# Optimization experiments

Measured on AMD Instinct MI355X. Metric: run time of the kernel, lower is better.

The kernel has to match this reference:

```python
import jax, jax.numpy as jnp
import numpy as np

N_NODES = 100000


def _gcn_norm(edge_index, num_nodes):
    """Add self-loops and compute symmetric GCN normalization coefficients.
    Returns (src, dst, norm) for the augmented edge list."""
    loop = jnp.arange(num_nodes, dtype=edge_index.dtype)
    src = jnp.concatenate([edge_index[0], loop])
    dst = jnp.concatenate([edge_index[1], loop])
    deg = jax.ops.segment_sum(jnp.ones_like(src, dtype=jnp.float32), dst,
                              num_segments=num_nodes)
    dinv = jnp.where(deg > 0, jax.lax.rsqrt(deg), 0.0)
    norm = dinv[src] * dinv[dst]  # [E + N]
    return src, dst, norm


def setup_inputs() -> dict:
    key = jax.random.key(0)
    ks = jax.random.split(key, 7)
    d = 64
    E = 1000000
    x = jax.random.normal(ks[0], (N_NODES, d), dtype=jnp.float32)
    edge_index = jax.random.randint(ks[1], (2, E), 0, N_NODES, dtype=jnp.int64)
    s = 1.0 / np.sqrt(d)
    Ws = jax.random.normal(ks[2], (3, d, d), dtype=jnp.float32) * s
    bs = jax.random.normal(ks[3], (3, d), dtype=jnp.float32) * 0.02
    W_out = jax.random.normal(ks[4], (d, d), dtype=jnp.float32) * s
    b_out = jax.random.normal(ks[5], (d,), dtype=jnp.float32) * 0.02
    return {"x": x, "edge_index": edge_index, "Ws": Ws, "bs": bs,
            "W_out": W_out, "b_out": b_out}


def reference(x, edge_index, Ws, bs, W_out, b_out):
    num_nodes = x.shape[0]
    src, dst, norm = _gcn_norm(edge_index, num_nodes)  # fixed graph -> compute once
    for i in range(Ws.shape[0]):  # small fixed layer count
        h = x @ Ws[i]                              # [N, d] linear transform
        msg = norm[:, None] * h[src]               # gather + scale  [E+N, d]
        x = jax.ops.segment_sum(msg, dst, num_segments=num_nodes) + bs[i]
        x = jax.nn.relu(x)
    return x @ W_out + b_out
```

## Files before the change

kernel.cpp:

```cpp
#include <hip/hip_runtime.h>
#include <hip/hip_bf16.h>

#define D 64
#define BSHIFT 8
#define BNODES 256
#define BCAP 4096
#define PTILE 2048

typedef __attribute__((ext_vector_type(8))) short short8;
typedef __attribute__((ext_vector_type(4))) float float4v;


__device__ __forceinline__ float bf16u_to_f32(unsigned short u) {
  union { unsigned int i; float f; } c;
  c.i = ((unsigned int)u) << 16;
  return c.f;
}

__device__ __forceinline__ unsigned short f32_to_bf16u(float f) {
  union { float f; unsigned int u; } c;
  c.f = f;
  unsigned int r = (c.u + 0x7fffu + ((c.u >> 16) & 1u)) >> 16;
  return (unsigned short)r;
}


__global__ void k_probe(const void* W, const void* ei, int* flags) {
  int lane = threadIdx.x & 63;
  const unsigned short* wb = (const unsigned short*)W;
  bool big = false;
  for (int i = lane; i < 512; i += 64) {
    float v = bf16u_to_f32(wb[i]);
    if (!(fabsf(v) < 100.f)) big = true;
  }
  int anybig = __any(big);
  const int* e32 = (const int*)ei;
  bool nz = (e32[2 * lane + 1] != 0);
  int anynz = __any(nz);
  if (threadIdx.x == 0) {
    flags[0] = anybig ? 1 : 0;
    flags[1] = anynz ? 0 : 1;
  }
}


__global__ __launch_bounds__(256) void k_prep(
    const void* __restrict__ Ws, const void* __restrict__ Wout,
    const void* __restrict__ bs, const void* __restrict__ bout,
    const int* __restrict__ flags, unsigned short* __restrict__ WT,
    float* __restrict__ biasf, int* __restrict__ bucket_cursor) {
  int f32 = flags[0];
  int gid = blockIdx.x * 256 + threadIdx.x;
  int stride = gridDim.x * 256;

  for (int i = gid; i < 512; i += stride) bucket_cursor[i] = i * BCAP;

  for (int i = gid; i < 4 * 4096; i += stride) {
    int l = i >> 12;
    int r = i & 4095;
    int k = r >> 6;
    int nn = r & 63;
    unsigned short v;
    if (l < 3) {
      v = f32 ? f32_to_bf16u(((const float*)Ws)[l * 4096 + r])
              : ((const unsigned short*)Ws)[l * 4096 + r];
    } else {
      v = f32 ? f32_to_bf16u(((const float*)Wout)[r])
              : ((const unsigned short*)Wout)[r];
    }
    WT[l * 4096 + nn * 64 + k] = v;
  }
  for (int i = gid; i < 4 * 64; i += stride) {
    int l = i >> 6;
    int j = i & 63;
    float v;
    if (l < 3)
      v = f32 ? ((const float*)bs)[l * 64 + j]
              : bf16u_to_f32(((const unsigned short*)bs)[l * 64 + j]);
    else
      v = f32 ? ((const float*)bout)[j]
              : bf16u_to_f32(((const unsigned short*)bout)[j]);
    biasf[i] = v;
  }
}


__global__ __launch_bounds__(256) void k_partition(
    const void* __restrict__ ei, const int* __restrict__ flags,
    int* __restrict__ bucket_cursor, int* __restrict__ packed, int e) {
  __shared__ int lhist[512];
  __shared__ int lbase[512];
  int tid = threadIdx.x;
  int t0 = blockIdx.x * PTILE;
  int tend = min(t0 + PTILE, e);
  if (t0 >= e) return;
  int i64 = flags[1];

  for (int b = tid; b < 512; b += 256) lhist[b] = 0;
  __syncthreads();

  if (i64) {
    const long long* dst = (const long long*)ei + e;
    for (int i = t0 + tid; i < tend; i += 256)
      atomicAdd(&lhist[((int)dst[i]) >> BSHIFT], 1);
  } else {
    const int* dst = (const int*)ei + e;
    for (int i = t0 + tid; i < tend; i += 256)
      atomicAdd(&lhist[dst[i] >> BSHIFT], 1);
  }
  __syncthreads();

  for (int b = tid; b < 512; b += 256) {
    int c = lhist[b];
    lbase[b] = c ? atomicAdd(&bucket_cursor[b], c) : 0;
    lhist[b] = 0;
  }
  __syncthreads();

  if (i64) {
    const long long* srcp = (const long long*)ei;
    const long long* dstp = srcp + e;
    for (int i = t0 + tid; i < tend; i += 256) {
      int s = (int)srcp[i];
      int d = (int)dstp[i];
      int b = d >> BSHIFT;
      int r = atomicAdd(&lhist[b], 1);
      packed[lbase[b] + r] = (s << BSHIFT) | (d & (BNODES - 1));
    }
  } else {
    const int* srcp = (const int*)ei;
    const int* dstp = srcp + e;
    for (int i = t0 + tid; i < tend; i += 256) {
      int s = srcp[i];
      int d = dstp[i];
      int b = d >> BSHIFT;
      int r = atomicAdd(&lhist[b], 1);
      packed[lbase[b] + r] = (s << BSHIFT) | (d & (BNODES - 1));
    }
  }
}

__global__ __launch_bounds__(256) void k_sort_csr(
    const int* __restrict__ packed, const int* __restrict__ bucket_cursor,
    int* __restrict__ csr, int2* __restrict__ rowrange,
    float* __restrict__ dinv, int n) {
  __shared__ int lcnt[BNODES];
  __shared__ int lofs[BNODES];
  __shared__ int sbuf[BNODES];
  int tid = threadIdx.x;
  int bucket = blockIdx.x;
  int node0 = bucket << BSHIFT;
  int nodes = min(BNODES, n - node0);
  int s0 = bucket * BCAP;
  int s1 = bucket_cursor[bucket];
  lcnt[tid] = 0;
  __syncthreads();
  for (int i = s0 + tid; i < s1; i += 256)
    atomicAdd(&lcnt[packed[i] & (BNODES - 1)], 1);
  __syncthreads();
  int v = lcnt[tid];
  sbuf[tid] = v;
  __syncthreads();
  for (int off = 1; off < BNODES; off <<= 1) {
    int tv = (tid >= off) ? sbuf[tid - off] : 0;
    __syncthreads();
    sbuf[tid] += tv;
    __syncthreads();
  }
  int excl = sbuf[tid] - v;
  lofs[tid] = excl;
  lcnt[tid] = 0;
  if (tid < nodes) {
    rowrange[node0 + tid] = make_int2(s0 + excl, s0 + excl + v);
    dinv[node0 + tid] = rsqrtf((float)(v + 1));
  }
  __syncthreads();
  for (int i = s0 + tid; i < s1; i += 256) {
    int pk = packed[i];
    int ld = pk & (BNODES - 1);
    int r = atomicAdd(&lcnt[ld], 1);
    csr[s0 + lofs[ld] + r] = pk >> BSHIFT;
  }
}


__global__ __launch_bounds__(256) void k_scale(
    const void* __restrict__ x0, const int* __restrict__ flags,
    const float* __restrict__ dinv, ushort4* __restrict__ z, int n16) {
  int f32 = flags[0];
  int i = blockIdx.x * 256 + threadIdx.x;
  int stride = gridDim.x * 256;
  for (; i < n16; i += stride) {
    float d = dinv[i >> 4];
    ushort4 o;
    if (f32) {
      float4 v = ((const float4*)x0)[i];
      o.x = f32_to_bf16u(d * v.x);
      o.y = f32_to_bf16u(d * v.y);
      o.z = f32_to_bf16u(d * v.z);
      o.w = f32_to_bf16u(d * v.w);
    } else {
      ushort4 v = ((const ushort4*)x0)[i];
      o.x = f32_to_bf16u(d * bf16u_to_f32(v.x));
      o.y = f32_to_bf16u(d * bf16u_to_f32(v.y));
      o.z = f32_to_bf16u(d * bf16u_to_f32(v.z));
      o.w = f32_to_bf16u(d * bf16u_to_f32(v.w));
    }
    z[i] = o;
  }
}

__global__ __launch_bounds__(256, 4) void k_fused(
    const unsigned short* __restrict__ z, const int2* __restrict__ rowrange,
    const int* __restrict__ csr, const float* __restrict__ dinv,
    const unsigned short* __restrict__ WT, const float* __restrict__ biasf,
    unsigned short* __restrict__ out, int n, int scale_out) {
  __shared__ unsigned short ybf[16 * 80];
  int tid = threadIdx.x;
  int lane = tid & 63;
  int w = tid >> 6;
  int q = lane >> 4;
  int f = lane & 15;
  int h = lane & 7;
  int g8 = lane >> 3;

  short8 b0 = *(const short8*)(WT + (size_t)(f + 16 * w) * 64 + q * 8);
  short8 b1 = *(const short8*)(WT + (size_t)(f + 16 * w) * 64 + 32 + q * 8);

  int row0 = blockIdx.x * 16;
  int base_node = row0 + w * 4;
  const short8* z8 = (const short8*)z;

  int rrw = 0;
  if (lane < 8) rrw = ((const int*)rowrange)[(size_t)base_node * 2 + lane];
  int rx0 = __shfl(rrw, 0, 64);
  int ry0 = __shfl(rrw, 1, 64);
  int rx1 = __shfl(rrw, 2, 64);
  int ry1 = __shfl(rrw, 3, 64);
  int rx2 = __shfl(rrw, 4, 64);
  int ry2 = __shfl(rrw, 5, 64);
  int rx3 = __shfl(rrw, 6, 64);
  int ry3 = __shfl(rrw, 7, 64);
  int deg0 = ry0 - rx0;
  int deg1 = ry1 - rx1;
  int deg2 = ry2 - rx2;
  int deg3 = ry3 - rx3;

  int jx = lane >> 4;
  int m = lane & 15;
  int rxj = (jx & 2) ? ((jx & 1) ? rx3 : rx2) : ((jx & 1) ? rx1 : rx0);
  int dgj = (jx & 2) ? ((jx & 1) ? deg3 : deg2) : ((jx & 1) ? deg1 : deg0);
  int coff = (m >= 1 && m <= dgj) ? (m - 1) : 0;
  int idx = csr[rxj + coff];
  if (m == 0) idx = base_node + jx;

  float ac[4][4][2];
  float a0[8] = {0, 0, 0, 0, 0, 0, 0, 0};
  float a1[8] = {0, 0, 0, 0, 0, 0, 0, 0};
  float a2[8] = {0, 0, 0, 0, 0, 0, 0, 0};
  float a3[8] = {0, 0, 0, 0, 0, 0, 0, 0};
  (void)ac;

  short8 g[8];
#pragma unroll
  for (int t = 0; t < 8; t++) {
    int u = ((t & 1) << 3) + g8;
    int sl = ((t >> 1) << 4) + u;
    int s = __shfl(idx, sl, 64);
    g[t] = z8[(size_t)s * 8 + h];
  }
#pragma unroll
  for (int t = 0; t < 8; t++) {
    int u = ((t & 1) << 3) + g8;
    const int j = t >> 1;
    int dg = (j == 0) ? deg0 : (j == 1) ? deg1 : (j == 2) ? deg2 : deg3;
    float vm = (u <= dg) ? 1.f : 0.f;
    float* aj = (j == 0) ? a0 : (j == 1) ? a1 : (j == 2) ? a2 : a3;
#pragma unroll
    for (int c = 0; c < 8; c++)
      aj[c] += vm * bf16u_to_f32((unsigned short)g[t][c]);
  }

#pragma unroll
  for (int j = 0; j < 4; j++) {
    int rx = (j == 0) ? rx0 : (j == 1) ? rx1 : (j == 2) ? rx2 : rx3;
    int dg = (j == 0) ? deg0 : (j == 1) ? deg1 : (j == 2) ? deg2 : deg3;
    float* aj = (j == 0) ? a0 : (j == 1) ? a1 : (j == 2) ? a2 : a3;
    for (int e0 = 15; e0 < dg; e0 += 8) {
      int e = e0 + g8;
      bool vv = e < dg;
      int s = csr[rx + (vv ? e : 0)];
      short8 tv = z8[(size_t)s * 8 + h];
      float vm = vv ? 1.f : 0.f;
#pragma unroll
      for (int c = 0; c < 8; c++)
        aj[c] += vm * bf16u_to_f32((unsigned short)tv[c]);
    }
  }

#pragma unroll
  for (int c = 0; c < 8; c++) {
    a0[c] += __shfl_xor(a0[c], 8, 64);
    a1[c] += __shfl_xor(a1[c], 8, 64);
    a2[c] += __shfl_xor(a2[c], 8, 64);
    a3[c] += __shfl_xor(a3[c], 8, 64);
    a0[c] += __shfl_xor(a0[c], 16, 64);
    a1[c] += __shfl_xor(a1[c], 16, 64);
    a2[c] += __shfl_xor(a2[c], 16, 64);
    a3[c] += __shfl_xor(a3[c], 16, 64);
    a0[c] += __shfl_xor(a0[c], 32, 64);
    a1[c] += __shfl_xor(a1[c], 32, 64);
    a2[c] += __shfl_xor(a2[c], 32, 64);
    a3[c] += __shfl_xor(a3[c], 32, 64);
  }

  if (lane < 32) {
    int jw = lane >> 3;
    float dv = dinv[base_node + jw];
    unsigned int pk[4];
#pragma unroll
    for (int cp = 0; cp < 4; cp++) {
      float vlo = (jw & 2) ? ((jw & 1) ? a3[2 * cp] : a2[2 * cp])
                           : ((jw & 1) ? a1[2 * cp] : a0[2 * cp]);
      float vhi = (jw & 2) ? ((jw & 1) ? a3[2 * cp + 1] : a2[2 * cp + 1])
                           : ((jw & 1) ? a1[2 * cp + 1] : a0[2 * cp + 1]);
      unsigned int lo = f32_to_bf16u(dv * vlo);
      unsigned int hi = f32_to_bf16u(dv * vhi);
      pk[cp] = lo | (hi << 16);
    }
    *(uint4*)&ybf[(w * 4 + jw) * 80 + 8 * h] =
        make_uint4(pk[0], pk[1], pk[2], pk[3]);
  }
  __syncthreads();

  short8 fa0 = *(const short8*)&ybf[f * 80 + q * 8];
  short8 fa1 = *(const short8*)&ybf[f * 80 + 32 + q * 8];
  float4v zz = {0.f, 0.f, 0.f, 0.f};
  float4v acc = __builtin_amdgcn_mfma_f32_16x16x32_bf16(fa0, b0, zz, 0, 0, 0);
  acc = __builtin_amdgcn_mfma_f32_16x16x32_bf16(fa1, b1, acc, 0, 0, 0);

  float bv = biasf[16 * w + f];
  if (scale_out) {
    float4 dv4 = *(const float4*)(dinv + row0 + q * 4);
    float d[4] = {dv4.x, dv4.y, dv4.z, dv4.w};
#pragma unroll
    for (int reg = 0; reg < 4; reg++) {
      int row = row0 + q * 4 + reg;
      if (row < n)
        out[(size_t)row * 64 + 16 * w + f] =
            f32_to_bf16u(d[reg] * fmaxf(acc[reg] + bv, 0.f));
    }
  } else {
#pragma unroll
    for (int reg = 0; reg < 4; reg++) {
      int row = row0 + q * 4 + reg;
      if (row < n)
        out[(size_t)row * 64 + 16 * w + f] =
            f32_to_bf16u(fmaxf(acc[reg] + bv, 0.f));
    }
  }
}

__global__ __launch_bounds__(256) void k_gemm_final(
    const unsigned short* __restrict__ xin,
    const unsigned short* __restrict__ WT, const float* __restrict__ bias,
    void* __restrict__ out, const int* __restrict__ flags, int ntiles) {
  int lane = threadIdx.x & 63;
  int wid = threadIdx.x >> 6;
  int f = lane & 15;
  int q = lane >> 4;

  short8 bfr[4][2];
#pragma unroll
  for (int ct = 0; ct < 4; ct++)
#pragma unroll
    for (int kt = 0; kt < 2; kt++)
      bfr[ct][kt] =
          *(const short8*)(WT + (size_t)(f + 16 * ct) * 64 + kt * 32 + q * 8);

  int wave = blockIdx.x * 4 + wid;
  int nwaves = gridDim.x * 4;
  for (int t = wave; t < ntiles; t += nwaves) {
    int row0 = t * 16;
    const unsigned short* xr = xin + (size_t)(row0 + f) * 64 + q * 8;
    short8 a0 = *(const short8*)(xr);
    short8 a1 = *(const short8*)(xr + 32);
    float4v acc[4];
#pragma unroll
    for (int ct = 0; ct < 4; ct++) {
      float4v z = {0.f, 0.f, 0.f, 0.f};
      acc[ct] =
          __builtin_amdgcn_mfma_f32_16x16x32_bf16(a0, bfr[ct][0], z, 0, 0, 0);
      acc[ct] = __builtin_amdgcn_mfma_f32_16x16x32_bf16(a1, bfr[ct][1],
                                                        acc[ct], 0, 0, 0);
    }
    int f32o = flags[0];
    float bv[4];
#pragma unroll
    for (int ct = 0; ct < 4; ct++) bv[ct] = bias[f + 16 * ct];
    if (f32o) {
      float* op = (float*)out;
#pragma unroll
      for (int reg = 0; reg < 4; reg++) {
        size_t rb = (size_t)(row0 + q * 4 + reg) * 64 + f;
#pragma unroll
        for (int ct = 0; ct < 4; ct++) op[rb + 16 * ct] = acc[ct][reg] + bv[ct];
      }
    } else {
      unsigned short* op = (unsigned short*)out;
#pragma unroll
      for (int reg = 0; reg < 4; reg++) {
        size_t rb = (size_t)(row0 + q * 4 + reg) * 64 + f;
#pragma unroll
        for (int ct = 0; ct < 4; ct++)
          op[rb + 16 * ct] = f32_to_bf16u(acc[ct][reg] + bv[ct]);
      }
    }
  }
}


extern "C" void kernel_launch(void* const* d_in, const int* in_sizes, int n_in,
                              void* d_out, int out_size, void* d_ws,
                              size_t ws_size, hipStream_t stream) {
  const void* x0 = d_in[0];
  const void* ei = d_in[1];
  const void* Ws = d_in[2];
  const void* bs = d_in[3];
  const void* Wout = d_in[4];
  const void* bout = d_in[5];

  const int N = in_sizes[0] / D;
  const int E = in_sizes[1] / 2;
  const int NBUC = (N + BNODES - 1) >> BSHIFT;
  const int NT = (N + 15) / 16;

  char* p = (char*)d_ws;
  auto alloc = [&](size_t bytes) {
    char* r = p;
    p += (bytes + 511) & ~(size_t)511;
    return r;
  };
  int* flags = (int*)alloc(8);
  int* bucket_cursor = (int*)alloc(512 * 4);
  int* packed = (int*)alloc((size_t)512 * BCAP * 4);
  int* csr = (int*)alloc((size_t)512 * BCAP * 4);
  int2* rowrange = (int2*)alloc((size_t)N * 8);
  float* dinv = (float*)alloc((size_t)N * 4);
  unsigned short* WT = (unsigned short*)alloc(4 * 4096 * 2);
  float* biasf = (float*)alloc(4 * 64 * 4);
  unsigned short* za = (unsigned short*)alloc((size_t)N * D * 2);
  unsigned short* zb = (unsigned short*)alloc((size_t)N * D * 2);
  (void)ws_size;
  (void)n_in;
  (void)out_size;

  k_probe<<<1, 64, 0, stream>>>(Ws, ei, flags);
  k_prep<<<32, 256, 0, stream>>>(Ws, Wout, bs, bout, flags, WT, biasf,
                                 bucket_cursor);
  int ptiles = (E + PTILE - 1) / PTILE;
  k_partition<<<ptiles, 256, 0, stream>>>(ei, flags, bucket_cursor, packed, E);
  k_sort_csr<<<NBUC, 256, 0, stream>>>(packed, bucket_cursor, csr, rowrange,
                                       dinv, N);
  k_scale<<<1024, 256, 0, stream>>>(x0, flags, dinv, (ushort4*)za, N * 16);

  k_fused<<<NT, 256, 0, stream>>>(za, rowrange, csr, dinv, WT + 0 * 4096,
                                  biasf + 0 * 64, zb, N, 1);
  k_fused<<<NT, 256, 0, stream>>>(zb, rowrange, csr, dinv, WT + 1 * 4096,
                                  biasf + 1 * 64, za, N, 1);
  k_fused<<<NT, 256, 0, stream>>>(za, rowrange, csr, dinv, WT + 2 * 4096,
                                  biasf + 2 * 64, zb, N, 0);
  k_gemm_final<<<(NT + 3) / 4, 256, 0, stream>>>(zb, WT + 3 * 4096,
                                                 biasf + 3 * 64, d_out, flags,
                                                 NT);
}
```

Measured before the change: 243.6 us.

## Make fused GCN layer kernel persistent with prefetch of next tile's row ranges

Turns the per-tile aggregation+GEMM kernel into a persistent grid-stride kernel with 1024 blocks. Each block prefetches and decodes the next tile's row ranges and neighbor indices while working on the current tile, and double-buffers the shared staging array. It also skips the upper-half gathers for nodes with degree under 8. The aim is to cut launch and block-scheduling overhead and hide index-load latency. In exchange, fewer blocks may lower latency hiding across the gather-heavy work, and register pressure rises.

```diff
diff --git a/kernel.cpp b/kernel.cpp
--- a/kernel.cpp
+++ b/kernel.cpp
@@ -214,150 +214,183 @@
     const unsigned short* __restrict__ z, const int2* __restrict__ rowrange,
     const int* __restrict__ csr, const float* __restrict__ dinv,
     const unsigned short* __restrict__ WT, const float* __restrict__ biasf,
-    unsigned short* __restrict__ out, int n, int scale_out) {
-  __shared__ unsigned short ybf[16 * 80];
-  int tid = threadIdx.x;
-  int lane = tid & 63;
-  int w = tid >> 6;
-  int q = lane >> 4;
-  int f = lane & 15;
-  int h = lane & 7;
-  int g8 = lane >> 3;
+    unsigned short* __restrict__ out, int n, int scale_out, int ntiles) {
+  __shared__ unsigned short ybf[2][16 * 80];
+  const int tid = threadIdx.x;
+  const int lane = tid & 63;
+  const int w = tid >> 6;
+  const int q = lane >> 4;
+  const int f = lane & 15;
+  const int h = lane & 7;
+  const int g8 = lane >> 3;
+  const int jx = lane >> 4;
+  const int m = lane & 15;
 
   short8 b0 = *(const short8*)(WT + (size_t)(f + 16 * w) * 64 + q * 8);
   short8 b1 = *(const short8*)(WT + (size_t)(f + 16 * w) * 64 + 32 + q * 8);
-
-  int row0 = blockIdx.x * 16;
-  int base_node = row0 + w * 4;
+  const float bv = biasf[16 * w + f];
+
   const short8* z8 = (const short8*)z;
+  const int NB = gridDim.x;
+  if ((int)blockIdx.x >= ntiles) return;
+
+  auto decode = [&](int rrw_v, int bn, int& rx0, int& rx1, int& rx2, int& rx3,
+                    int& d0, int& d1, int& d2, int& d3) -> int {
+    rx0 = __shfl(rrw_v, 0, 64);
+    int ry0 = __shfl(rrw_v, 1, 64);
+    rx1 = __shfl(rrw_v, 2, 64);
+    int ry1 = __shfl(rrw_v, 3, 64);
+    rx2 = __shfl(rrw_v, 4, 64);
+    int ry2 = __shfl(rrw_v, 5, 64);
+    rx3 = __shfl(rrw_v, 6, 64);
+    int ry3 = __shfl(rrw_v, 7, 64);
+    d0 = ry0 - rx0;
+    d1 = ry1 - rx1;
+    d2 = ry2 - rx2;
+    d3 = ry3 - rx3;
+    int rxj = (jx & 2) ? ((jx & 1) ? rx3 : rx2) : ((jx & 1) ? rx1 : rx0);
+    int dgj = (jx & 2) ? ((jx & 1) ? d3 : d2) : ((jx & 1) ? d1 : d0);
+    int coff = (m >= 1 && m <= dgj) ? (m - 1) : 0;
+    int idxv = csr[rxj + coff];
+    if (m == 0) idxv = bn + jx;
+    return idxv;
+  };
 
   int rrw = 0;
-  if (lane < 8) rrw = ((const int*)rowrange)[(size_t)base_node * 2 + lane];
-  int rx0 = __shfl(rrw, 0, 64);
-  int ry0 = __shfl(rrw, 1, 64);
-  int rx1 = __shfl(rrw, 2, 64);
-  int ry1 = __shfl(rrw, 3, 64);
-  int rx2 = __shfl(rrw, 4, 64);
-  int ry2 = __shfl(rrw, 5, 64);
-  int rx3 = __shfl(rrw, 6, 64);
-  int ry3 = __shfl(rrw, 7, 64);
-  int deg0 = ry0 - rx0;
-  int deg1 = ry1 - rx1;
-  int deg2 = ry2 - rx2;
-  int deg3 = ry3 - rx3;
-
-  int jx = lane >> 4;
-  int m = lane & 15;
-  int rxj = (jx & 2) ? ((jx & 1) ? rx3 : rx2) : ((jx & 1) ? rx1 : rx0);
-  int dgj = (jx & 2) ? ((jx & 1) ? deg3 : deg2) : ((jx & 1) ? deg1 : deg0);
-  int coff = (m >= 1 && m <= dgj) ? (m - 1) : 0;
-  int idx = csr[rxj + coff];
-  if (m == 0) idx = base_node + jx;
-
-  float ac[4][4][2];
-  float a0[8] = {0, 0, 0, 0, 0, 0, 0, 0};
-  float a1[8] = {0, 0, 0, 0, 0, 0, 0, 0};
-  float a2[8] = {0, 0, 0, 0, 0, 0, 0, 0};
-  float a3[8] = {0, 0, 0, 0, 0, 0, 0, 0};
-  (void)ac;
-
-  short8 g[8];
-#pragma unroll
-  for (int t = 0; t < 8; t++) {
-    int u = ((t & 1) << 3) + g8;
-    int sl = ((t >> 1) << 4) + u;
-    int s = __shfl(idx, sl, 64);
-    g[t] = z8[(size_t)s * 8 + h];
-  }
-#pragma unroll
-  for (int t = 0; t < 8; t++) {
-    int u = ((t & 1) << 3) + g8;
-    const int j = t >> 1;
-    int dg = (j == 0) ? deg0 : (j == 1) ? deg1 : (j == 2) ? deg2 : deg3;
-    float vm = (u <= dg) ? 1.f : 0.f;
-    float* aj = (j == 0) ? a0 : (j == 1) ? a1 : (j == 2) ? a2 : a3;
-#pragma unroll
-    for (int c = 0; c < 8; c++)
-      aj[c] += vm * bf16u_to_f32((unsigned short)g[t][c]);
-  }
-
-#pragma unroll
-  for (int j = 0; j < 4; j++) {
-    int rx = (j == 0) ? rx0 : (j == 1) ? rx1 : (j == 2) ? rx2 : rx3;
-    int dg = (j == 0) ? deg0 : (j == 1) ? deg1 : (j == 2) ? deg2 : deg3;
-    float* aj = (j == 0) ? a0 : (j == 1) ? a1 : (j == 2) ? a2 : a3;
-    for (int e0 = 15; e0 < dg; e0 += 8) {
-      int e = e0 + g8;
-      bool vv = e < dg;
-      int s = csr[rx + (vv ? e : 0)];
-      short8 tv = z8[(size_t)s * 8 + h];
-      float vm = vv ? 1.f : 0.f;
+  if (lane < 8)
+    rrw = ((const int*)rowrange)[((size_t)blockIdx.x * 16 + w * 4) * 2 + lane];
+  int rx0, rx1, rx2, rx3, d0, d1, d2, d3;
+  int idx = decode(rrw, blockIdx.x * 16 + w * 4, rx0, rx1, rx2, rx3, d0, d1,
+                   d2, d3);
+  int pp = 0;
+
+  for (int t = blockIdx.x; t < ntiles; t += NB) {
+    const int tn = t + NB;
+    const int row0 = t * 16;
+    const int base_node = row0 + w * 4;
+
+    int rrw_n = 0;
+    if (lane < 8 && tn < ntiles)
+      rrw_n = ((const int*)rowrange)[((size_t)tn * 16 + w * 4) * 2 + lane];
+
+    short8 g[8];
+#pragma unroll
+    for (int t8 = 0; t8 < 8; t8++) {
+      const int j = t8 >> 1;
+      const int hi = t8 & 1;
+      int dg = (j == 0) ? d0 : (j == 1) ? d1 : (j == 2) ? d2 : d3;
+      if (hi && dg < 8) continue;
+      int u = (hi << 3) + g8;
+      int s = __shfl(idx, (j << 4) + u, 64);
+      g[t8] = z8[(size_t)s * 8 + h];
+    }
+
+    float a0[8] = {0, 0, 0, 0, 0, 0, 0, 0};
+    float a1[8] = {0, 0, 0, 0, 0, 0, 0, 0};
+    float a2[8] = {0, 0, 0, 0, 0, 0, 0, 0};
+    float a3[8] = {0, 0, 0, 0, 0, 0, 0, 0};
+#pragma unroll
+    for (int t8 = 0; t8 < 8; t8++) {
+      const int j = t8 >> 1;
+      const int hi = t8 & 1;
+      int dg = (j == 0) ? d0 : (j == 1) ? d1 : (j == 2) ? d2 : d3;
+      if (hi && dg < 8) continue;
+      int u = (hi << 3) + g8;
+      float vm = (u <= dg) ? 1.f : 0.f;
+      float* aj = (j == 0) ? a0 : (j == 1) ? a1 : (j == 2) ? a2 : a3;
 #pragma unroll
       for (int c = 0; c < 8; c++)
-        aj[c] += vm * bf16u_to_f32((unsigned short)tv[c]);
-    }
-  }
-
-#pragma unroll
-  for (int c = 0; c < 8; c++) {
-    a0[c] += __shfl_xor(a0[c], 8, 64);
-    a1[c] += __shfl_xor(a1[c], 8, 64);
-    a2[c] += __shfl_xor(a2[c], 8, 64);
-    a3[c] += __shfl_xor(a3[c], 8, 64);
-    a0[c] += __shfl_xor(a0[c], 16, 64);
-    a1[c] += __shfl_xor(a1[c], 16, 64);
-    a2[c] += __shfl_xor(a2[c], 16, 64);
-    a3[c] += __shfl_xor(a3[c], 16, 64);
-    a0[c] += __shfl_xor(a0[c], 32, 64);
-    a1[c] += __shfl_xor(a1[c], 32, 64);
-    a2[c] += __shfl_xor(a2[c], 32, 64);
-    a3[c] += __shfl_xor(a3[c], 32, 64);
-  }
-
-  if (lane < 32) {
-    int jw = lane >> 3;
-    float dv = dinv[base_node + jw];
-    unsigned int pk[4];
-#pragma unroll
-    for (int cp = 0; cp < 4; cp++) {
-      float vlo = (jw & 2) ? ((jw & 1) ? a3[2 * cp] : a2[2 * cp])
-                           : ((jw & 1) ? a1[2 * cp] : a0[2 * cp]);
-      float vhi = (jw & 2) ? ((jw & 1) ? a3[2 * cp + 1] : a2[2 * cp + 1])
-                           : ((jw & 1) ? a1[2 * cp + 1] : a0[2 * cp + 1]);
-      unsigned int lo = f32_to_bf16u(dv * vlo);
-      unsigned int hi = f32_to_bf16u(dv * vhi);
-      pk[cp] = lo | (hi << 16);
-    }
-    *(uint4*)&ybf[(w * 4 + jw) * 80 + 8 * h] =
-        make_uint4(pk[0], pk[1], pk[2], pk[3]);
-  }
-  __syncthreads();
-
-  short8 fa0 = *(const short8*)&ybf[f * 80 + q * 8];
-  short8 fa1 = *(const short8*)&ybf[f * 80 + 32 + q * 8];
-  float4v zz = {0.f, 0.f, 0.f, 0.f};
-  float4v acc = __builtin_amdgcn_mfma_f32_16x16x32_bf16(fa0, b0, zz, 0, 0, 0);
-  acc = __builtin_amdgcn_mfma_f32_16x16x32_bf16(fa1, b1, acc, 0, 0, 0);
-
-  float bv = biasf[16 * w + f];
-  if (scale_out) {
-    float4 dv4 = *(const float4*)(dinv + row0 + q * 4);
-    float d[4] = {dv4.x, dv4.y, dv4.z, dv4.w};
-#pragma unroll
-    for (int reg = 0; reg < 4; reg++) {
-      int row = row0 + q * 4 + reg;
-      if (row < n)
-        out[(size_t)row * 64 + 16 * w + f] =
-            f32_to_bf16u(d[reg] * fmaxf(acc[reg] + bv, 0.f));
-    }
-  } else {
-#pragma unroll
-    for (int reg = 0; reg < 4; reg++) {
-      int row = row0 + q * 4 + reg;
-      if (row < n)
-        out[(size_t)row * 64 + 16 * w + f] =
-            f32_to_bf16u(fmaxf(acc[reg] + bv, 0.f));
-    }
+        aj[c] += vm * bf16u_to_f32((unsigned short)g[t8][c]);
+    }
+
+    int nrx0 = 0, nrx1 = 0, nrx2 = 0, nrx3 = 0;
+    int nd0 = 0, nd1 = 0, nd2 = 0, nd3 = 0, idx_n = 0;
+    if (tn < ntiles)
+      idx_n = decode(rrw_n, tn * 16 + w * 4, nrx0, nrx1, nrx2, nrx3, nd0, nd1,
+                     nd2, nd3);
+
+#pragma unroll
+    for (int j = 0; j < 4; j++) {
+      int rx = (j == 0) ? rx0 : (j == 1) ? rx1 : (j == 2) ? rx2 : rx3;
+      int dg = (j == 0) ? d0 : (j == 1) ? d1 : (j == 2) ? d2 : d3;
+      float* aj = (j == 0) ? a0 : (j == 1) ? a1 : (j == 2) ? a2 : a3;
+      for (int e0 = 15; e0 < dg; e0 += 8) {
+        int e = e0 + g8;
+        bool vv = e < dg;
+        int s = csr[rx + (vv ? e : 0)];
+        short8 tv = z8[(size_t)s * 8 + h];
+        float vm = vv ? 1.f : 0.f;
+#pragma unroll
+        for (int c = 0; c < 8; c++)
+          aj[c] += vm * bf16u_to_f32((unsigned short)tv[c]);
+      }
+    }
+
+#pragma unroll
+    for (int c = 0; c < 8; c++) {
+      a0[c] += __shfl_xor(a0[c], 8, 64);
+      a1[c] += __shfl_xor(a1[c], 8, 64);
+      a2[c] += __shfl_xor(a2[c], 8, 64);
+      a3[c] += __shfl_xor(a3[c], 8, 64);
+      a0[c] += __shfl_xor(a0[c], 16, 64);
+      a1[c] += __shfl_xor(a1[c], 16, 64);
+      a2[c] += __shfl_xor(a2[c], 16, 64);
+      a3[c] += __shfl_xor(a3[c], 16, 64);
+      a0[c] += __shfl_xor(a0[c], 32, 64);
+      a1[c] += __shfl_xor(a1[c], 32, 64);
+      a2[c] += __shfl_xor(a2[c], 32, 64);
+      a3[c] += __shfl_xor(a3[c], 32, 64);
+    }
+
+    if (lane < 32) {
+      int jw = lane >> 3;
+      float dv = dinv[base_node + jw];
+      unsigned int pk[4];
+#pragma unroll
+      for (int cp = 0; cp < 4; cp++) {
+        float vlo = (jw & 2) ? ((jw & 1) ? a3[2 * cp] : a2[2 * cp])
+                             : ((jw & 1) ? a1[2 * cp] : a0[2 * cp]);
+        float vhi = (jw & 2) ? ((jw & 1) ? a3[2 * cp + 1] : a2[2 * cp + 1])
+                             : ((jw & 1) ? a1[2 * cp + 1] : a0[2 * cp + 1]);
+        unsigned int lo = f32_to_bf16u(dv * vlo);
+        unsigned int hi = f32_to_bf16u(dv * vhi);
+        pk[cp] = lo | (hi << 16);
+      }
+      *(uint4*)&ybf[pp][(w * 4 + jw) * 80 + 8 * h] =
+          make_uint4(pk[0], pk[1], pk[2], pk[3]);
+    }
+    __syncthreads();
+
+    short8 fa0 = *(const short8*)&ybf[pp][f * 80 + q * 8];
+    short8 fa1 = *(const short8*)&ybf[pp][f * 80 + 32 + q * 8];
+    float4v zz = {0.f, 0.f, 0.f, 0.f};
+    float4v acc = __builtin_amdgcn_mfma_f32_16x16x32_bf16(fa0, b0, zz, 0, 0, 0);
+    acc = __builtin_amdgcn_mfma_f32_16x16x32_bf16(fa1, b1, acc, 0, 0, 0);
+
+    if (scale_out) {
+      float4 dv4 = *(const float4*)(dinv + row0 + q * 4);
+      float dvr[4] = {dv4.x, dv4.y, dv4.z, dv4.w};
+#pragma unroll
+      for (int reg = 0; reg < 4; reg++) {
+        int row = row0 + q * 4 + reg;
+        if (row < n)
+          out[(size_t)row * 64 + 16 * w + f] =
+              f32_to_bf16u(dvr[reg] * fmaxf(acc[reg] + bv, 0.f));
+      }
+    } else {
+#pragma unroll
+      for (int reg = 0; reg < 4; reg++) {
+        int row = row0 + q * 4 + reg;
+        if (row < n)
+          out[(size_t)row * 64 + 16 * w + f] =
+              f32_to_bf16u(fmaxf(acc[reg] + bv, 0.f));
+      }
+    }
+
+    rx0 = nrx0; rx1 = nrx1; rx2 = nrx2; rx3 = nrx3;
+    d0 = nd0; d1 = nd1; d2 = nd2; d3 = nd3;
+    idx = idx_n;
+    pp ^= 1;
   }
 }
 
@@ -464,12 +497,13 @@
                                        dinv, N);
   k_scale<<<1024, 256, 0, stream>>>(x0, flags, dinv, (ushort4*)za, N * 16);
 
-  k_fused<<<NT, 256, 0, stream>>>(za, rowrange, csr, dinv, WT + 0 * 4096,
-                                  biasf + 0 * 64, zb, N, 1);
-  k_fused<<<NT, 256, 0, stream>>>(zb, rowrange, csr, dinv, WT + 1 * 4096,
-                                  biasf + 1 * 64, za, N, 1);
-  k_fused<<<NT, 256, 0, stream>>>(za, rowrange, csr, dinv, WT + 2 * 4096,
-                                  biasf + 2 * 64, zb, N, 0);
+  const int FGRID = 1024;
+  k_fused<<<FGRID, 256, 0, stream>>>(za, rowrange, csr, dinv, WT + 0 * 4096,
+                                     biasf + 0 * 64, zb, N, 1, NT);
+  k_fused<<<FGRID, 256, 0, stream>>>(zb, rowrange, csr, dinv, WT + 1 * 4096,
+                                     biasf + 1 * 64, za, N, 1, NT);
+  k_fused<<<FGRID, 256, 0, stream>>>(za, rowrange, csr, dinv, WT + 2 * 4096,
+                                     biasf + 2 * 64, zb, N, 0, NT);
   k_gemm_final<<<(NT + 3) / 4, 256, 0, stream>>>(zb, WT + 3 * 4096,
                                                  biasf + 3 * 64, d_out, flags,
                                                  NT);
```

New measurement: 262.1 us. 1.08x slower.
